# Optimization experiments

Hardware: AMD Instinct MI355X
Metric: run time of the kernel (lower is better)

## Reference

```python
import jax, jax.numpy as jnp
import numpy as np

B, S, D = 2, 1024, 768
H, DH = 12, 64
M = 64            # performer random features
DFF = 4 * D
EPS_LN = 1e-5
EPS_PHI = 1e-6


def setup_inputs() -> dict:
    key = jax.random.key(0)
    ks = jax.random.split(key, 12)
    std = 0.02
    return {
        "x": jax.random.normal(ks[0], (B, S, D), jnp.float32),
        "ln1_g": jnp.ones((D,), jnp.float32),
        "ln1_b": jnp.zeros((D,), jnp.float32),
        "w_attn": jax.random.normal(ks[1], (D, 3 * D), jnp.float32) * std,
        "b_attn": jnp.zeros((3 * D,), jnp.float32),
        "w_feat": jax.random.normal(ks[2], (M, DH), jnp.float32),  # FAVOR+ projection
        "w_proj": jax.random.normal(ks[3], (D, D), jnp.float32) * std,
        "b_proj": jnp.zeros((D,), jnp.float32),
        "ln2_g": jnp.ones((D,), jnp.float32),
        "ln2_b": jnp.zeros((D,), jnp.float32),
        "w_fc": jax.random.normal(ks[4], (D, DFF), jnp.float32) * std,
        "b_fc": jnp.zeros((DFF,), jnp.float32),
        "w_out": jax.random.normal(ks[5], (DFF, D), jnp.float32) * std,
        "b_out": jnp.zeros((D,), jnp.float32),
    }


def _layernorm(x, g, b):
    mu = jnp.mean(x, axis=-1, keepdims=True)
    var = jnp.mean(jnp.square(x - mu), axis=-1, keepdims=True)
    return (x - mu) * jax.lax.rsqrt(var + EPS_LN) * g + b


def _phi(x, w_feat):
    # FAVOR+ positive softmax-kernel features. x: [B,H,S,DH] (already scaled by dh^-1/4)
    proj = jnp.einsum('bhsd,md->bhsm', x, w_feat)
    sq = 0.5 * jnp.sum(jnp.square(x), axis=-1, keepdims=True)
    return jnp.exp(proj - sq) / np.sqrt(M) + EPS_PHI


def _performer_attn(q, k, v, w_feat, w_proj, b_proj):
    # split heads: [B,S,D] -> [B,H,S,DH]
    def heads(t):
        return t.reshape(B, S, H, DH).transpose(0, 2, 1, 3)
    q, k, v = heads(q), heads(k), heads(v)
    scale = DH ** -0.25
    phi_q = _phi(q * scale, w_feat)  # [B,H,S,M]
    phi_k = _phi(k * scale, w_feat)
    # causal linear attention via prefix sums
    kv = jnp.cumsum(phi_k[..., :, None] * v[..., None, :], axis=2)  # [B,H,S,M,DH]
    num = jnp.einsum('bhsm,bhsmd->bhsd', phi_q, kv)
    den = jnp.einsum('bhsm,bhsm->bhs', phi_q, jnp.cumsum(phi_k, axis=2))
    out = num / den[..., None]
    out = out.transpose(0, 2, 1, 3).reshape(B, S, D)
    return out @ w_proj + b_proj


def reference(x, ln1_g, ln1_b, w_attn, b_attn, w_feat, w_proj, b_proj,
              ln2_g, ln2_b, w_fc, b_fc, w_out, b_out):
    a = _layernorm(x, ln1_g, ln1_b)
    qkv = a @ w_attn + b_attn                      # TFConv1D
    q, k, v = jnp.split(qkv, 3, axis=2)
    x = x + _performer_attn(q, k, v, w_feat, w_proj, b_proj)
    m = _layernorm(x, ln2_g, ln2_b)
    m = jax.nn.gelu(m @ w_fc + b_fc, approximate=True) @ w_out + b_out
    return x + m
```

## Files before the change

kernel.cpp:

```cpp
#include <hip/hip_runtime.h>
#include <hip/hip_bf16.h>
#include <math.h>

#define BB 2
#define SS 1024
#define DD 768
#define HH 12
#define DHH 64
#define MM 64
#define DFF 3072
#define BS (BB*SS)
#define EPS_LN 1e-5f
#define EPS_PHI 1e-6f
#define CC 64
#define NC (SS/CC)
#define NQ 3840
#define PQOFF 2304
#define PKOFF 3072
#define VOFF  1536

typedef __hip_bfloat16 bf16;
using v8s = __attribute__((ext_vector_type(8))) short;
using v4f = __attribute__((ext_vector_type(4))) float;
struct b4 { bf16 v[4]; };

typedef const __attribute__((address_space(1))) void ga_void;
typedef __attribute__((address_space(3))) void ls_void;
__device__ __forceinline__ void gload16(const void* g, void* l) {
    __builtin_amdgcn_global_load_lds((ga_void*)g, (ls_void*)l, 16, 0, 0);
}

__global__ __launch_bounds__(256) void feat_kernel(const float* __restrict__ w_attn,
                                                   const float* __restrict__ b_attn,
                                                   const float* __restrict__ wfeat,
                                                   bf16* __restrict__ wext_t,
                                                   float* __restrict__ bias_ext) {
    __shared__ float wfTm[64][68];
    __shared__ float Wt[64][68];
    int bid = blockIdx.x;
    int t = threadIdx.x;
    if (bid == 288) {
        for (int i = t; i < 3 * DD; i += 256) bias_ext[i] = b_attn[i];
        return;
    }
    int jb = bid % 12, h = (bid / 12) % 12, isK = bid / 144;
    int j0 = jb * 64;
    int base = isK * DD + h * DHH;
    const float scale = 0.35355339059327373f;
    #pragma unroll
    for (int it = 0; it < 4; it++) {
        int fidx = it * 256 + t;
        int r = fidx >> 4, dc = (fidx & 15) * 4;
        float4 wv = *(const float4*)&wfeat[r * DHH + dc];
        wfTm[r][dc + 0] = scale * wv.x; wfTm[r][dc + 1] = scale * wv.y;
        wfTm[r][dc + 2] = scale * wv.z; wfTm[r][dc + 3] = scale * wv.w;
        float4 av = *(const float4*)&w_attn[(size_t)(j0 + r) * (3 * DD) + base + dc];
        Wt[r][dc + 0] = av.x; Wt[r][dc + 1] = av.y;
        Wt[r][dc + 2] = av.z; Wt[r][dc + 3] = av.w;
    }
    __syncthreads();
    int jl = t & 63, mg = (t >> 6) * 16;
    v4f acc[16];
    #pragma unroll
    for (int mi = 0; mi < 16; mi++) acc[mi] = {0.f, 0.f, 0.f, 0.f};
    #pragma unroll
    for (int dc = 0; dc < 16; dc++) {
        v4f wv = *(const v4f*)&Wt[jl][dc * 4];
        #pragma unroll
        for (int mi = 0; mi < 16; mi++) {
            v4f fv = *(const v4f*)&wfTm[mg + mi][dc * 4];
            acc[mi] += fv * wv;
        }
    }
    #pragma unroll
    for (int mi = 0; mi < 16; mi++) {
        float s = acc[mi][0] + acc[mi][1] + acc[mi][2] + acc[mi][3];
        wext_t[(size_t)(PQOFF + isK * DD + h * DHH + mg + mi) * DD + j0 + jl] = __float2bfloat16(s);
    }
    if (jb == 0 && t < 64) {
        float accb = 0.f;
        #pragma unroll 8
        for (int d = 0; d < 64; d++) accb += wfTm[t][d] * b_attn[base + d];
        bias_ext[PQOFF + isK * DD + h * DHH + t] = accb;
    }
}

__global__ __launch_bounds__(256) void prep_main(const float* __restrict__ x,
                                                 const float* __restrict__ ln1_g,
                                                 const float* __restrict__ ln1_b,
                                                 const float* __restrict__ w_attn,
                                                 const float* __restrict__ w_proj,
                                                 const float* __restrict__ w_fc,
                                                 const float* __restrict__ w_out,
                                                 bf16* __restrict__ a_bf,
                                                 bf16* __restrict__ wext_t,
                                                 bf16* __restrict__ wproj_t,
                                                 bf16* __restrict__ wfc_t,
                                                 bf16* __restrict__ wout_t) {
    __shared__ float smem[64 * 65];
    int bid = blockIdx.x;
    int t = threadIdx.x;
    if (bid < 2048) {
        int row = bid;
        const float* xr = x + (size_t)row * DD;
        float v0 = xr[t], v1 = xr[t + 256], v2 = xr[t + 512];
        float s = v0 + v1 + v2;
        float s2 = v0 * v0 + v1 * v1 + v2 * v2;
        #pragma unroll
        for (int off = 32; off > 0; off >>= 1) {
            s  += __shfl_xor(s,  off, 64);
            s2 += __shfl_xor(s2, off, 64);
        }
        float* ls = smem; float* ls2 = smem + 4;
        if ((t & 63) == 0) { ls[t >> 6] = s; ls2[t >> 6] = s2; }
        __syncthreads();
        s  = ls[0] + ls[1] + ls[2] + ls[3];
        s2 = ls2[0] + ls2[1] + ls2[2] + ls2[3];
        float mu  = s * (1.0f / DD);
        float var = s2 * (1.0f / DD) - mu * mu;
        float r = rsqrtf(var + EPS_LN);
        bf16* orow = a_bf + (size_t)row * DD;
        orow[t]       = __float2bfloat16((v0 - mu) * r * ln1_g[t]       + ln1_b[t]);
        orow[t + 256] = __float2bfloat16((v1 - mu) * r * ln1_g[t + 256] + ln1_b[t + 256]);
        orow[t + 512] = __float2bfloat16((v2 - mu) * r * ln1_g[t + 512] + ln1_b[t + 512]);
    } else {
        int b = bid - 2048;
        const float* in; bf16* outp; int K, N, xt, yt;
        if (b < 432)       { in = w_attn; outp = wext_t;  K = 768;  N = 2304; xt = b % 36; yt = b / 36; }
        else if (b < 576)  { int b1 = b - 432;  in = w_proj; outp = wproj_t; K = 768;  N = 768;  xt = b1 % 12; yt = b1 / 12; }
        else if (b < 1152) { int b1 = b - 576;  in = w_fc;   outp = wfc_t;   K = 768;  N = 3072; xt = b1 % 48; yt = b1 / 48; }
        else               { int b1 = b - 1152; in = w_out;  outp = wout_t;  K = 3072; N = 768;  xt = b1 % 12; yt = b1 / 12; }
        float (*sm)[65] = (float(*)[65])smem;
        int n0 = xt * 64, k0 = yt * 64;
        int rr = t >> 4, cc = (t & 15) * 4;
        #pragma unroll
        for (int it = 0; it < 4; it++) {
            int kr = it * 16 + rr;
            float4 v = *(const float4*)&in[(size_t)(k0 + kr) * N + n0 + cc];
            sm[kr][cc + 0] = v.x; sm[kr][cc + 1] = v.y;
            sm[kr][cc + 2] = v.z; sm[kr][cc + 3] = v.w;
        }
        __syncthreads();
        #pragma unroll
        for (int it = 0; it < 4; it++) {
            int nr = it * 16 + rr;
            b4 o;
            #pragma unroll
            for (int j = 0; j < 4; j++) o.v[j] = __float2bfloat16(sm[cc + j][nr]);
            *(b4*)&outp[(size_t)(n0 + nr) * K + k0 + cc] = o;
        }
    }
}

__global__ __launch_bounds__(256) void ln_kernel(const float* __restrict__ x,
                                                 const float* __restrict__ g,
                                                 const float* __restrict__ bta,
                                                 bf16* __restrict__ out) {
    int row = blockIdx.x;
    int t = threadIdx.x;
    const float* xr = x + (size_t)row * DD;
    float v0 = xr[t], v1 = xr[t + 256], v2 = xr[t + 512];
    float s = v0 + v1 + v2;
    float s2 = v0 * v0 + v1 * v1 + v2 * v2;
    #pragma unroll
    for (int off = 32; off > 0; off >>= 1) {
        s  += __shfl_xor(s,  off, 64);
        s2 += __shfl_xor(s2, off, 64);
    }
    __shared__ float ls[4], ls2[4];
    if ((t & 63) == 0) { ls[t >> 6] = s; ls2[t >> 6] = s2; }
    __syncthreads();
    s  = ls[0] + ls[1] + ls[2] + ls[3];
    s2 = ls2[0] + ls2[1] + ls2[2] + ls2[3];
    float mu  = s * (1.0f / DD);
    float var = s2 * (1.0f / DD) - mu * mu;
    float r = rsqrtf(var + EPS_LN);
    bf16* orow = out + (size_t)row * DD;
    orow[t]       = __float2bfloat16((v0 - mu) * r * g[t]       + bta[t]);
    orow[t + 256] = __float2bfloat16((v1 - mu) * r * g[t + 256] + bta[t + 256]);
    orow[t + 512] = __float2bfloat16((v2 - mu) * r * g[t + 512] + bta[t + 512]);
}

__device__ inline void swizzle44(int bid, int nx4, int& bx, int& by) {
    int g = bid >> 4, r = bid & 15;
    bx = (g % nx4) * 4 + (r & 3);
    by = (g / nx4) * 4 + (r >> 2);
}

__device__ inline float gelu_tanh(float x) {
    float x3 = x * x * x;
    float u = 0.7978845608028654f * (x + 0.044715f * x3);
    return 0.5f * x * (1.0f + tanhf(u));
}

template <int ACT, int HAS_RES, int OUT_BF16, int SQMODE>
__global__ __launch_bounds__(256) void gemm_k128(const bf16* __restrict__ A,
                                                 const bf16* __restrict__ BT,
                                                 const float* __restrict__ bias,
                                                 const float* __restrict__ res,
                                                 void* __restrict__ Cout,
                                                 int N, int K, int nx4,
                                                 float* __restrict__ sqbuf) {
    __shared__ bf16 Asl[64][128];
    __shared__ bf16 Bsl[64][128];
    int bx, by;
    swizzle44(blockIdx.x, nx4, bx, by);
    int tid = threadIdx.x;
    int m0 = by * 64, n0 = bx * 64;
    int wave = tid >> 6, lane = tid & 63;
    int qm = lane & 15, quad = lane >> 4;
    int srow = lane >> 4;
    int chnk = lane & 15;
    int sce = (chnk ^ srow) * 8;
    int sco = (chnk ^ (srow + 4)) * 8;
    const bf16* ag = A  + (size_t)(m0 + wave * 16 + srow) * K;
    const bf16* bg = BT + (size_t)(n0 + wave * 16 + srow) * K;
    int xr = (qm & 7) << 3;

    v4f acc[4] = {{0.f,0.f,0.f,0.f},{0.f,0.f,0.f,0.f},{0.f,0.f,0.f,0.f},{0.f,0.f,0.f,0.f}};

    for (int k0 = 0; k0 < K; k0 += 128) {
        __syncthreads();
        #pragma unroll
        for (int i = 0; i < 4; i++) {
            int sc = (i & 1) ? sco : sce;
            gload16(ag + (size_t)(4 * i) * K + k0 + sc, &Asl[wave * 16 + 4 * i][0]);
            gload16(bg + (size_t)(4 * i) * K + k0 + sc, &Bsl[wave * 16 + 4 * i][0]);
        }
        __syncthreads();
        #pragma unroll
        for (int kc = 0; kc < 4; kc++) {
            v8s a = *(const v8s*)&Asl[wave * 16 + qm][(kc * 32 + quad * 8) ^ xr];
            #pragma unroll
            for (int n = 0; n < 4; n++) {
                v8s b = *(const v8s*)&Bsl[n * 16 + qm][(kc * 32 + quad * 8) ^ xr];
                acc[n] = __builtin_amdgcn_mfma_f32_16x16x32_bf16(a, b, acc[n], 0, 0, 0);
            }
        }
    }

    int col_l = lane & 15;
    if (SQMODE && n0 < 1536) {
        int hidx = n0 >> 6;
        #pragma unroll
        for (int r = 0; r < 4; r++) {
            float hsq = 0.f;
            #pragma unroll
            for (int t2 = 0; t2 < 4; t2++) {
                float v = acc[t2][r] + bias[n0 + t2 * 16 + col_l];
                hsq += v * v;
            }
            hsq += __shfl_xor(hsq, 1, 64); hsq += __shfl_xor(hsq, 2, 64);
            hsq += __shfl_xor(hsq, 4, 64); hsq += __shfl_xor(hsq, 8, 64);
            if (col_l == 0) {
                int row = m0 + wave * 16 + quad * 4 + r;
                sqbuf[row * 24 + hidx] = hsq * (1.0f / 16.0f);
            }
        }
        return;
    }
    #pragma unroll
    for (int t2 = 0; t2 < 4; t2++) {
        int col = n0 + t2 * 16 + col_l;
        float bcol = bias[col];
        #pragma unroll
        for (int r = 0; r < 4; r++) {
            int row = m0 + wave * 16 + quad * 4 + r;
            float v = acc[t2][r] + bcol;
            if (ACT == 1) v = gelu_tanh(v);
            if (HAS_RES) v += res[(size_t)row * N + col];
            if (OUT_BF16) ((bf16*)Cout)[(size_t)row * N + col] = __float2bfloat16(v);
            else          ((float*)Cout)[(size_t)row * N + col] = v;
        }
    }
}

template <int ACT, int HAS_RES, int OUT_BF16>
__global__ __launch_bounds__(256) void gemm_m32_k128(const bf16* __restrict__ A,
                                                     const bf16* __restrict__ BT,
                                                     const float* __restrict__ bias,
                                                     const float* __restrict__ res,
                                                     void* __restrict__ Cout,
                                                     int N, int K, int nx4) {
    __shared__ bf16 Asl[32][128];
    __shared__ bf16 Bsl[64][128];
    int bx, by;
    swizzle44(blockIdx.x, nx4, bx, by);
    int tid = threadIdx.x;
    int m0 = by * 32, n0 = bx * 64;
    int wave = tid >> 6, lane = tid & 63;
    int qm = lane & 15, quad = lane >> 4;
    int rowh = (wave & 1) * 16;
    int colh = (wave >> 1) * 32;
    int srow = lane >> 4;
    int chnk = lane & 15;
    int sce = (chnk ^ srow) * 8;
    int sco = (chnk ^ (srow + 4)) * 8;
    const bf16* ag = A  + (size_t)(m0 + wave * 8  + srow) * K;
    const bf16* bg = BT + (size_t)(n0 + wave * 16 + srow) * K;
    int xr = (qm & 7) << 3;

    v4f acc[2] = {{0.f,0.f,0.f,0.f},{0.f,0.f,0.f,0.f}};

    for (int k0 = 0; k0 < K; k0 += 128) {
        __syncthreads();
        #pragma unroll
        for (int i = 0; i < 2; i++) {
            int sc = (i & 1) ? sco : sce;
            gload16(ag + (size_t)(4 * i) * K + k0 + sc, &Asl[wave * 8 + 4 * i][0]);
        }
        #pragma unroll
        for (int i = 0; i < 4; i++) {
            int sc = (i & 1) ? sco : sce;
            gload16(bg + (size_t)(4 * i) * K + k0 + sc, &Bsl[wave * 16 + 4 * i][0]);
        }
        __syncthreads();
        #pragma unroll
        for (int kc = 0; kc < 4; kc++) {
            v8s a  = *(const v8s*)&Asl[rowh + qm][(kc * 32 + quad * 8) ^ xr];
            v8s b0 = *(const v8s*)&Bsl[colh + qm][(kc * 32 + quad * 8) ^ xr];
            v8s b1 = *(const v8s*)&Bsl[colh + 16 + qm][(kc * 32 + quad * 8) ^ xr];
            acc[0] = __builtin_amdgcn_mfma_f32_16x16x32_bf16(a, b0, acc[0], 0, 0, 0);
            acc[1] = __builtin_amdgcn_mfma_f32_16x16x32_bf16(a, b1, acc[1], 0, 0, 0);
        }
    }

    #pragma unroll
    for (int ct = 0; ct < 2; ct++) {
        int col = n0 + colh + ct * 16 + qm;
        float bcol = bias[col];
        #pragma unroll
        for (int r = 0; r < 4; r++) {
            int row = m0 + rowh + quad * 4 + r;
            float v = acc[ct][r] + bcol;
            if (ACT == 1) v = gelu_tanh(v);
            if (HAS_RES) v += res[(size_t)row * N + col];
            if (OUT_BF16) ((bf16*)Cout)[(size_t)row * N + col] = __float2bfloat16(v);
            else          ((float*)Cout)[(size_t)row * N + col] = v;
        }
    }
}

__global__ __launch_bounds__(256) void scan_sums_mfma(const bf16* __restrict__ qkvp,
                                                      const float* __restrict__ sqbuf,
                                                      float* __restrict__ StateT,
                                                      float* __restrict__ Sk) {
    int c = blockIdx.x, h = blockIdx.y, b = blockIdx.z;
    int bh = b * HH + h;
    int t = threadIdx.x;
    __shared__ bf16 vt[64][72];
    __shared__ bf16 kt[64][72];
    int sr = t >> 4, cq = (t & 15) * 4;
    #pragma unroll
    for (int i = 0; i < 4; i++) {
        int s = sr + 16 * i;
        size_t grow = (size_t)b * SS + c * CC + s;
        size_t rowg = grow * NQ + h * DHH;
        b4 vv = *(const b4*)&qkvp[rowg + VOFF  + cq];
        b4 kp = *(const b4*)&qkvp[rowg + PKOFF + cq];
        float sq = sqbuf[grow * 24 + 12 + h];
        #pragma unroll
        for (int j = 0; j < 4; j++) {
            vt[cq + j][s] = vv.v[j];
            kt[cq + j][s] = __float2bfloat16(
                __expf(__bfloat162float(kp.v[j]) - sq) * 0.125f + EPS_PHI);
        }
    }
    __syncthreads();
    int wave = t >> 6, lane = t & 63, qm = lane & 15, quad = lane >> 4;
    v4f acc[4] = {{0.f,0.f,0.f,0.f},{0.f,0.f,0.f,0.f},{0.f,0.f,0.f,0.f},{0.f,0.f,0.f,0.f}};
    #pragma unroll
    for (int k0 = 0; k0 < 64; k0 += 32) {
        v8s a = *(const v8s*)&vt[wave * 16 + qm][k0 + quad * 8];
        #pragma unroll
        for (int n = 0; n < 4; n++) {
            v8s bb = *(const v8s*)&kt[n * 16 + qm][k0 + quad * 8];
            acc[n] = __builtin_amdgcn_mfma_f32_16x16x32_bf16(a, bb, acc[n], 0, 0, 0);
        }
    }
    float* dst = StateT + ((size_t)bh * NC + c) * 4096;
    int col_l = lane & 15;
    #pragma unroll
    for (int n = 0; n < 4; n++)
        #pragma unroll
        for (int r = 0; r < 4; r++) {
            int d = wave * 16 + quad * 4 + r;
            dst[d * 64 + n * 16 + col_l] = acc[n][r];
        }
    {
        int m = t >> 2, j = t & 3;
        float sum = 0.f;
        #pragma unroll
        for (int i2 = 0; i2 < 16; i2++) sum += __bfloat162float(kt[m][j * 16 + i2]);
        sum += __shfl_xor(sum, 1, 64);
        sum += __shfl_xor(sum, 2, 64);
        if (j == 0) Sk[((size_t)bh * NC + c) * 64 + m] = sum;
    }
}

__global__ __launch_bounds__(256) void scan_prefix_kernel(float* __restrict__ Skv,
                                                          float* __restrict__ Sk) {
    int bh = blockIdx.y;
    int t = blockIdx.x * 256 + threadIdx.x;
    size_t base = (size_t)bh * NC * 4096 + t;
    float acc = 0.f;
    for (int c = 0; c < NC; c++) {
        float v = Skv[base + (size_t)c * 4096];
        Skv[base + (size_t)c * 4096] = acc;
        acc += v;
    }
    if (blockIdx.x == 0 && threadIdx.x < 64) {
        size_t b2 = (size_t)bh * NC * 64 + threadIdx.x;
        float a2 = 0.f;
        for (int c = 0; c < NC; c++) {
            float v = Sk[b2 + (size_t)c * 64];
            Sk[b2 + (size_t)c * 64] = a2;
            a2 += v;
        }
    }
}

__global__ __launch_bounds__(256) void scan_chunk_mfma(const bf16* __restrict__ qkvp,
                                                       const float* __restrict__ sqbuf,
                                                       const float* __restrict__ StateT,
                                                       const float* __restrict__ SkPre,
                                                       bf16* __restrict__ attn) {
    int c = blockIdx.x, h = blockIdx.y, b = blockIdx.z;
    int bh = b * HH + h;
    int t = threadIdx.x;
    __shared__ bf16 qs[64][72];
    __shared__ bf16 ks[64][72];
    __shared__ bf16 vt[64][72];
    __shared__ bf16 stl[64][72];
    __shared__ bf16 P[64][72];
    int sr = t >> 4, cq = (t & 15) * 4;
    const float* stg = StateT + ((size_t)bh * NC + c) * 4096;
    #pragma unroll
    for (int i = 0; i < 4; i++) {
        int s = sr + 16 * i;
        size_t grow = (size_t)b * SS + c * CC + s;
        size_t rowg = grow * NQ + h * DHH;
        b4 qp = *(const b4*)&qkvp[rowg + PQOFF + cq];
        b4 kp = *(const b4*)&qkvp[rowg + PKOFF + cq];
        b4 vv = *(const b4*)&qkvp[rowg + VOFF  + cq];
        float4 sv = *(const float4*)&stg[s * 64 + cq];
        float sqq = sqbuf[grow * 24 + h];
        float sqk = sqbuf[grow * 24 + 12 + h];
        #pragma unroll
        for (int j = 0; j < 4; j++) {
            qs[s][cq + j] = __float2bfloat16(
                __expf(__bfloat162float(qp.v[j]) - sqq) * 0.125f + EPS_PHI);
            ks[s][cq + j] = __float2bfloat16(
                __expf(__bfloat162float(kp.v[j]) - sqk) * 0.125f + EPS_PHI);
            vt[cq + j][s] = vv.v[j];
        }
        stl[s][cq + 0] = __float2bfloat16(sv.x);
        stl[s][cq + 1] = __float2bfloat16(sv.y);
        stl[s][cq + 2] = __float2bfloat16(sv.z);
        stl[s][cq + 3] = __float2bfloat16(sv.w);
    }
    __syncthreads();
    int wave = t >> 6, lane = t & 63, qm = lane & 15, quad = lane >> 4;
    int col_l = lane & 15;
    int row0 = wave * 16;

    v4f a1[4] = {{0.f,0.f,0.f,0.f},{0.f,0.f,0.f,0.f},{0.f,0.f,0.f,0.f},{0.f,0.f,0.f,0.f}};
    #pragma unroll
    for (int k0 = 0; k0 < 64; k0 += 32) {
        v8s a = *(const v8s*)&qs[row0 + qm][k0 + quad * 8];
        #pragma unroll
        for (int n = 0; n < 4; n++) {
            v8s bb = *(const v8s*)&ks[n * 16 + qm][k0 + quad * 8];
            a1[n] = __builtin_amdgcn_mfma_f32_16x16x32_bf16(a, bb, a1[n], 0, 0, 0);
        }
    }
    float denl[4] = {0.f, 0.f, 0.f, 0.f};
    #pragma unroll
    for (int n = 0; n < 4; n++)
        #pragma unroll
        for (int r = 0; r < 4; r++) {
            int row = row0 + quad * 4 + r;
            int col = n * 16 + col_l;
            float v = (col <= row) ? a1[n][r] : 0.f;
            P[row][col] = __float2bfloat16(v);
            denl[r] += v;
        }
    {
        const float* skp = SkPre + ((size_t)bh * NC + c) * 64;
        float4 sk4 = *(const float4*)&skp[qm * 4];
        #pragma unroll
        for (int r = 0; r < 4; r++) {
            int row = row0 + quad * 4 + r;
            b4 qv = *(const b4*)&qs[row][qm * 4];
            denl[r] += __bfloat162float(qv.v[0]) * sk4.x
                     + __bfloat162float(qv.v[1]) * sk4.y
                     + __bfloat162float(qv.v[2]) * sk4.z
                     + __bfloat162float(qv.v[3]) * sk4.w;
        }
    }
    #pragma unroll
    for (int r = 0; r < 4; r++) {
        denl[r] += __shfl_xor(denl[r], 1, 64);
        denl[r] += __shfl_xor(denl[r], 2, 64);
        denl[r] += __shfl_xor(denl[r], 4, 64);
        denl[r] += __shfl_xor(denl[r], 8, 64);
    }
    v4f acc[4] = {{0.f,0.f,0.f,0.f},{0.f,0.f,0.f,0.f},{0.f,0.f,0.f,0.f},{0.f,0.f,0.f,0.f}};
    #pragma unroll
    for (int k0 = 0; k0 < 64; k0 += 32) {
        v8s aq = *(const v8s*)&qs[row0 + qm][k0 + quad * 8];
        v8s ap = *(const v8s*)&P [row0 + qm][k0 + quad * 8];
        #pragma unroll
        for (int n = 0; n < 4; n++) {
            v8s b1 = *(const v8s*)&stl[n * 16 + qm][k0 + quad * 8];
            v8s b2 = *(const v8s*)&vt [n * 16 + qm][k0 + quad * 8];
            acc[n] = __builtin_amdgcn_mfma_f32_16x16x32_bf16(aq, b1, acc[n], 0, 0, 0);
            acc[n] = __builtin_amdgcn_mfma_f32_16x16x32_bf16(ap, b2, acc[n], 0, 0, 0);
        }
    }
    #pragma unroll
    for (int n = 0; n < 4; n++)
        #pragma unroll
        for (int r = 0; r < 4; r++) {
            int srow = row0 + quad * 4 + r;
            int d = n * 16 + col_l;
            attn[((size_t)b * SS + c * CC + srow) * DD + h * DHH + d] =
                __float2bfloat16(acc[n][r] / denl[r]);
        }
}

extern "C" void kernel_launch(void* const* d_in, const int* in_sizes, int n_in,
                              void* d_out, int out_size, void* d_ws, size_t ws_size,
                              hipStream_t stream) {
    const float* x      = (const float*)d_in[0];
    const float* ln1_g  = (const float*)d_in[1];
    const float* ln1_b  = (const float*)d_in[2];
    const float* w_attn = (const float*)d_in[3];
    const float* b_attn = (const float*)d_in[4];
    const float* w_feat = (const float*)d_in[5];
    const float* w_proj = (const float*)d_in[6];
    const float* b_proj = (const float*)d_in[7];
    const float* ln2_g  = (const float*)d_in[8];
    const float* ln2_b  = (const float*)d_in[9];
    const float* w_fc   = (const float*)d_in[10];
    const float* b_fc   = (const float*)d_in[11];
    const float* w_out  = (const float*)d_in[12];
    const float* b_out  = (const float*)d_in[13];
    float* out = (float*)d_out;

    float* ws = (float*)d_ws;
    size_t off = 0;
    float* buf_x1   = ws + off; off += (size_t)BS * DD;
    float* buf_sk   = ws + off; off += (size_t)BB * HH * NC * MM;
    float* bias_ext = ws + off; off += NQ;
    float* buf_sq   = ws + off; off += (size_t)BS * 24;
    bf16* wb = (bf16*)(ws + off);
    size_t boff = 0;
    bf16* buf_qkvp    = wb + boff; boff += (size_t)BS * NQ;
    bf16* buf_a_bf    = wb + boff; boff += (size_t)BS * DD;
    bf16* buf_attn_bf = wb + boff; boff += (size_t)BS * DD;
    bf16* wext_t      = wb + boff; boff += (size_t)NQ * DD;
    bf16* wproj_t     = wb + boff; boff += (size_t)DD * DD;
    bf16* wfc_t       = wb + boff; boff += (size_t)DFF * DD;
    bf16* wout_t      = wb + boff; boff += (size_t)DD * DFF;
    float* buf_skv   = buf_x1;
    bf16*  buf_fc_bf = buf_qkvp;

    feat_kernel<<<289, 256, 0, stream>>>(w_attn, b_attn, w_feat, wext_t, bias_ext);
    prep_main<<<3776, 256, 0, stream>>>(x, ln1_g, ln1_b,
                                        w_attn, w_proj, w_fc, w_out,
                                        buf_a_bf, wext_t, wproj_t, wfc_t, wout_t);
    gemm_k128<0, 0, 1, 1><<<1920, 256, 0, stream>>>(
        buf_a_bf, wext_t, bias_ext, nullptr, buf_qkvp, NQ, DD, 15, buf_sq);
    scan_sums_mfma<<<dim3(NC, HH, BB), 256, 0, stream>>>(buf_qkvp, buf_sq, buf_skv, buf_sk);
    scan_prefix_kernel<<<dim3(4096 / 256, BB * HH), 256, 0, stream>>>(buf_skv, buf_sk);
    scan_chunk_mfma<<<dim3(NC, HH, BB), 256, 0, stream>>>(
        buf_qkvp, buf_sq, buf_skv, buf_sk, buf_attn_bf);
    gemm_m32_k128<0, 1, 0><<<768, 256, 0, stream>>>(
        buf_attn_bf, wproj_t, b_proj, x, buf_x1, DD, DD, 3);
    ln_kernel<<<BS, 256, 0, stream>>>(buf_x1, ln2_g, ln2_b, buf_a_bf);
    gemm_k128<1, 0, 1, 0><<<1536, 256, 0, stream>>>(
        buf_a_bf, wfc_t, b_fc, nullptr, buf_fc_bf, DFF, DD, 12, nullptr);
    gemm_m32_k128<0, 1, 0><<<768, 256, 0, stream>>>(
        buf_fc_bf, wout_t, b_out, buf_x1, out, DD, DFF, 3);
}
```

Measured before the change: 211.4 us.

## Use 2x2 wave tiling in GEMM and fuse chunk prefix scan via last-block atomic

The 64x64 GEMM tile is now split into a 2x2 grid of 32x32 wave subtiles, so each wave loads two A and two B fragments per k-step instead of one A and four B. This cuts LDS reads per MFMA. Because each wave now covers only half a head's columns, the squared-norm side buffer stores two partial sums per head, and the consumers add them. Separately, the standalone prefix-scan kernel is removed: the last chunk block of each (batch, head), found with an atomic counter and threadfences, does the sequential prefix over chunk states itself. This saves a launch but puts a serial 16-chunk scan on a single block per head.

```diff
diff --git a/kernel.cpp b/kernel.cpp
--- a/kernel.cpp
+++ b/kernel.cpp
@@ -34,13 +34,15 @@
                                                    const float* __restrict__ b_attn,
                                                    const float* __restrict__ wfeat,
                                                    bf16* __restrict__ wext_t,
-                                                   float* __restrict__ bias_ext) {
+                                                   float* __restrict__ bias_ext,
+                                                   int* __restrict__ cnt) {
     __shared__ float wfTm[64][68];
     __shared__ float Wt[64][68];
     int bid = blockIdx.x;
     int t = threadIdx.x;
     if (bid == 288) {
         for (int i = t; i < 3 * DD; i += 256) bias_ext[i] = b_attn[i];
+        if (t < BB * HH) cnt[t] = 0;
         return;
     }
     int jb = bid % 12, h = (bid / 12) % 12, isK = bid / 144;
@@ -216,8 +218,10 @@
     const bf16* ag = A  + (size_t)(m0 + wave * 16 + srow) * K;
     const bf16* bg = BT + (size_t)(n0 + wave * 16 + srow) * K;
     int xr = (qm & 7) << 3;
-
-    v4f acc[4] = {{0.f,0.f,0.f,0.f},{0.f,0.f,0.f,0.f},{0.f,0.f,0.f,0.f},{0.f,0.f,0.f,0.f}};
+    int wr = (wave & 1) * 32, wc = (wave >> 1) * 32;
+
+    v4f acc[2][2] = {{{0.f,0.f,0.f,0.f},{0.f,0.f,0.f,0.f}},
+                     {{0.f,0.f,0.f,0.f},{0.f,0.f,0.f,0.f}}};
 
     for (int k0 = 0; k0 < K; k0 += 128) {
         __syncthreads();
@@ -230,47 +234,57 @@
         __syncthreads();
         #pragma unroll
         for (int kc = 0; kc < 4; kc++) {
-            v8s a = *(const v8s*)&Asl[wave * 16 + qm][(kc * 32 + quad * 8) ^ xr];
-            #pragma unroll
-            for (int n = 0; n < 4; n++) {
-                v8s b = *(const v8s*)&Bsl[n * 16 + qm][(kc * 32 + quad * 8) ^ xr];
-                acc[n] = __builtin_amdgcn_mfma_f32_16x16x32_bf16(a, b, acc[n], 0, 0, 0);
-            }
+            int off = (kc * 32 + quad * 8) ^ xr;
+            v8s a0 = *(const v8s*)&Asl[wr + qm][off];
+            v8s a1 = *(const v8s*)&Asl[wr + 16 + qm][off];
+            v8s b0 = *(const v8s*)&Bsl[wc + qm][off];
+            v8s b1 = *(const v8s*)&Bsl[wc + 16 + qm][off];
+            acc[0][0] = __builtin_amdgcn_mfma_f32_16x16x32_bf16(a0, b0, acc[0][0], 0, 0, 0);
+            acc[0][1] = __builtin_amdgcn_mfma_f32_16x16x32_bf16(a0, b1, acc[0][1], 0, 0, 0);
+            acc[1][0] = __builtin_amdgcn_mfma_f32_16x16x32_bf16(a1, b0, acc[1][0], 0, 0, 0);
+            acc[1][1] = __builtin_amdgcn_mfma_f32_16x16x32_bf16(a1, b1, acc[1][1], 0, 0, 0);
         }
     }
 
     int col_l = lane & 15;
     if (SQMODE && n0 < 1536) {
         int hidx = n0 >> 6;
-        #pragma unroll
-        for (int r = 0; r < 4; r++) {
-            float hsq = 0.f;
+        int half = wc >> 5;
+        #pragma unroll
+        for (int m = 0; m < 2; m++) {
             #pragma unroll
-            for (int t2 = 0; t2 < 4; t2++) {
-                float v = acc[t2][r] + bias[n0 + t2 * 16 + col_l];
-                hsq += v * v;
+            for (int r = 0; r < 4; r++) {
+                float hsq = 0.f;
+                #pragma unroll
+                for (int n = 0; n < 2; n++) {
+                    float v = acc[m][n][r] + bias[n0 + wc + n * 16 + col_l];
+                    hsq += v * v;
+                }
+                hsq += __shfl_xor(hsq, 1, 64); hsq += __shfl_xor(hsq, 2, 64);
+                hsq += __shfl_xor(hsq, 4, 64); hsq += __shfl_xor(hsq, 8, 64);
+                if (col_l == 0) {
+                    int row = m0 + wr + m * 16 + quad * 4 + r;
+                    sqbuf[(size_t)row * 48 + hidx * 2 + half] = hsq * (1.0f / 16.0f);
+                }
             }
-            hsq += __shfl_xor(hsq, 1, 64); hsq += __shfl_xor(hsq, 2, 64);
-            hsq += __shfl_xor(hsq, 4, 64); hsq += __shfl_xor(hsq, 8, 64);
-            if (col_l == 0) {
-                int row = m0 + wave * 16 + quad * 4 + r;
-                sqbuf[row * 24 + hidx] = hsq * (1.0f / 16.0f);
+        }
+        return;
+    }
+    #pragma unroll
+    for (int n = 0; n < 2; n++) {
+        int col = n0 + wc + n * 16 + col_l;
+        float bcol = bias[col];
+        #pragma unroll
+        for (int m = 0; m < 2; m++) {
+            #pragma unroll
+            for (int r = 0; r < 4; r++) {
+                int row = m0 + wr + m * 16 + quad * 4 + r;
+                float v = acc[m][n][r] + bcol;
+                if (ACT == 1) v = gelu_tanh(v);
+                if (HAS_RES) v += res[(size_t)row * N + col];
+                if (OUT_BF16) ((bf16*)Cout)[(size_t)row * N + col] = __float2bfloat16(v);
+                else          ((float*)Cout)[(size_t)row * N + col] = v;
             }
-        }
-        return;
-    }
-    #pragma unroll
-    for (int t2 = 0; t2 < 4; t2++) {
-        int col = n0 + t2 * 16 + col_l;
-        float bcol = bias[col];
-        #pragma unroll
-        for (int r = 0; r < 4; r++) {
-            int row = m0 + wave * 16 + quad * 4 + r;
-            float v = acc[t2][r] + bcol;
-            if (ACT == 1) v = gelu_tanh(v);
-            if (HAS_RES) v += res[(size_t)row * N + col];
-            if (OUT_BF16) ((bf16*)Cout)[(size_t)row * N + col] = __float2bfloat16(v);
-            else          ((float*)Cout)[(size_t)row * N + col] = v;
         }
     }
 }
@@ -344,12 +358,14 @@
 __global__ __launch_bounds__(256) void scan_sums_mfma(const bf16* __restrict__ qkvp,
                                                       const float* __restrict__ sqbuf,
                                                       float* __restrict__ StateT,
-                                                      float* __restrict__ Sk) {
+                                                      float* __restrict__ Sk,
+                                                      int* __restrict__ cnt) {
     int c = blockIdx.x, h = blockIdx.y, b = blockIdx.z;
     int bh = b * HH + h;
     int t = threadIdx.x;
     __shared__ bf16 vt[64][72];
     __shared__ bf16 kt[64][72];
+    __shared__ int lastFlag;
     int sr = t >> 4, cq = (t & 15) * 4;
     #pragma unroll
     for (int i = 0; i < 4; i++) {
@@ -358,7 +374,7 @@
         size_t rowg = grow * NQ + h * DHH;
         b4 vv = *(const b4*)&qkvp[rowg + VOFF  + cq];
         b4 kp = *(const b4*)&qkvp[rowg + PKOFF + cq];
-        float sq = sqbuf[grow * 24 + 12 + h];
+        float sq = sqbuf[grow * 48 + 24 + h * 2] + sqbuf[grow * 48 + 24 + h * 2 + 1];
         #pragma unroll
         for (int j = 0; j < 4; j++) {
             vt[cq + j][s] = vv.v[j];
@@ -396,25 +412,34 @@
         sum += __shfl_xor(sum, 2, 64);
         if (j == 0) Sk[((size_t)bh * NC + c) * 64 + m] = sum;
     }
-}
-
-__global__ __launch_bounds__(256) void scan_prefix_kernel(float* __restrict__ Skv,
-                                                          float* __restrict__ Sk) {
-    int bh = blockIdx.y;
-    int t = blockIdx.x * 256 + threadIdx.x;
-    size_t base = (size_t)bh * NC * 4096 + t;
-    float acc = 0.f;
-    for (int c = 0; c < NC; c++) {
-        float v = Skv[base + (size_t)c * 4096];
-        Skv[base + (size_t)c * 4096] = acc;
-        acc += v;
-    }
-    if (blockIdx.x == 0 && threadIdx.x < 64) {
-        size_t b2 = (size_t)bh * NC * 64 + threadIdx.x;
+    __threadfence();
+    if (t == 0) {
+        int old = atomicAdd(&cnt[bh], 1);
+        lastFlag = (old == NC - 1);
+    }
+    __syncthreads();
+    if (!lastFlag) return;
+    __threadfence();
+    float* base = StateT + (size_t)bh * NC * 4096;
+    float accp[16];
+    #pragma unroll
+    for (int i = 0; i < 16; i++) accp[i] = 0.f;
+    for (int c2 = 0; c2 < NC; c2++) {
+        float v[16];
+        #pragma unroll
+        for (int i = 0; i < 16; i++) v[i] = base[(size_t)c2 * 4096 + t + i * 256];
+        #pragma unroll
+        for (int i = 0; i < 16; i++) {
+            base[(size_t)c2 * 4096 + t + i * 256] = accp[i];
+            accp[i] += v[i];
+        }
+    }
+    if (t < 64) {
+        size_t b2 = (size_t)bh * NC * 64 + t;
         float a2 = 0.f;
-        for (int c = 0; c < NC; c++) {
-            float v = Sk[b2 + (size_t)c * 64];
-            Sk[b2 + (size_t)c * 64] = a2;
+        for (int c2 = 0; c2 < NC; c2++) {
+            float v = Sk[b2 + (size_t)c2 * 64];
+            Sk[b2 + (size_t)c2 * 64] = a2;
             a2 += v;
         }
     }
@@ -444,8 +469,8 @@
         b4 kp = *(const b4*)&qkvp[rowg + PKOFF + cq];
         b4 vv = *(const b4*)&qkvp[rowg + VOFF  + cq];
         float4 sv = *(const float4*)&stg[s * 64 + cq];
-        float sqq = sqbuf[grow * 24 + h];
-        float sqk = sqbuf[grow * 24 + 12 + h];
+        float sqq = sqbuf[grow * 48 + h * 2]      + sqbuf[grow * 48 + h * 2 + 1];
+        float sqk = sqbuf[grow * 48 + 24 + h * 2] + sqbuf[grow * 48 + 24 + h * 2 + 1];
         #pragma unroll
         for (int j = 0; j < 4; j++) {
             qs[s][cq + j] = __float2bfloat16(
@@ -553,7 +578,8 @@
     float* buf_x1   = ws + off; off += (size_t)BS * DD;
     float* buf_sk   = ws + off; off += (size_t)BB * HH * NC * MM;
     float* bias_ext = ws + off; off += NQ;
-    float* buf_sq   = ws + off; off += (size_t)BS * 24;
+    float* buf_sq   = ws + off; off += (size_t)BS * 48;
+    int*   buf_cnt  = (int*)(ws + off); off += 32;
     bf16* wb = (bf16*)(ws + off);
     size_t boff = 0;
     bf16* buf_qkvp    = wb + boff; boff += (size_t)BS * NQ;
@@ -566,14 +592,14 @@
     float* buf_skv   = buf_x1;
     bf16*  buf_fc_bf = buf_qkvp;
 
-    feat_kernel<<<289, 256, 0, stream>>>(w_attn, b_attn, w_feat, wext_t, bias_ext);
+    feat_kernel<<<289, 256, 0, stream>>>(w_attn, b_attn, w_feat, wext_t, bias_ext, buf_cnt);
     prep_main<<<3776, 256, 0, stream>>>(x, ln1_g, ln1_b,
                                         w_attn, w_proj, w_fc, w_out,
                                         buf_a_bf, wext_t, wproj_t, wfc_t, wout_t);
     gemm_k128<0, 0, 1, 1><<<1920, 256, 0, stream>>>(
         buf_a_bf, wext_t, bias_ext, nullptr, buf_qkvp, NQ, DD, 15, buf_sq);
-    scan_sums_mfma<<<dim3(NC, HH, BB), 256, 0, stream>>>(buf_qkvp, buf_sq, buf_skv, buf_sk);
-    scan_prefix_kernel<<<dim3(4096 / 256, BB * HH), 256, 0, stream>>>(buf_skv, buf_sk);
+    scan_sums_mfma<<<dim3(NC, HH, BB), 256, 0, stream>>>(
+        buf_qkvp, buf_sq, buf_skv, buf_sk, buf_cnt);
     scan_chunk_mfma<<<dim3(NC, HH, BB), 256, 0, stream>>>(
         buf_qkvp, buf_sq, buf_skv, buf_sk, buf_attn_bf);
     gemm_m32_k128<0, 1, 0><<<768, 256, 0, stream>>>(
```

Result: slower. 272.0 us (+28.7%).

## Use 2x2 wave tiling in the 64x64 GEMM to cut LDS fragment reads

Applied to the files above, without the earlier changes.

The GEMM's four waves now each compute a 32x32 quadrant of the 64x64 tile using a 2x2 grid of MFMA accumulators. Before, each wave computed a 16x64 strip. Per k-chunk this needs 4 LDS fragment loads for 4 MFMAs instead of 5, so LDS traffic drops. Because each wave now covers only half of a head's columns, the sum-of-squares epilogue writes two partial sums per head into a buffer twice as wide. The scan and attention kernels add the two halves when they read it.

```diff
diff --git a/kernel.cpp b/kernel.cpp
--- a/kernel.cpp
+++ b/kernel.cpp
@@ -216,8 +216,10 @@
     const bf16* ag = A  + (size_t)(m0 + wave * 16 + srow) * K;
     const bf16* bg = BT + (size_t)(n0 + wave * 16 + srow) * K;
     int xr = (qm & 7) << 3;
-
-    v4f acc[4] = {{0.f,0.f,0.f,0.f},{0.f,0.f,0.f,0.f},{0.f,0.f,0.f,0.f},{0.f,0.f,0.f,0.f}};
+    int wr = (wave & 1) * 32, wc = (wave >> 1) * 32;
+
+    v4f acc[2][2] = {{{0.f,0.f,0.f,0.f},{0.f,0.f,0.f,0.f}},
+                     {{0.f,0.f,0.f,0.f},{0.f,0.f,0.f,0.f}}};
 
     for (int k0 = 0; k0 < K; k0 += 128) {
         __syncthreads();
@@ -230,47 +232,57 @@
         __syncthreads();
         #pragma unroll
         for (int kc = 0; kc < 4; kc++) {
-            v8s a = *(const v8s*)&Asl[wave * 16 + qm][(kc * 32 + quad * 8) ^ xr];
-            #pragma unroll
-            for (int n = 0; n < 4; n++) {
-                v8s b = *(const v8s*)&Bsl[n * 16 + qm][(kc * 32 + quad * 8) ^ xr];
-                acc[n] = __builtin_amdgcn_mfma_f32_16x16x32_bf16(a, b, acc[n], 0, 0, 0);
-            }
+            int off = (kc * 32 + quad * 8) ^ xr;
+            v8s a0 = *(const v8s*)&Asl[wr + qm][off];
+            v8s a1 = *(const v8s*)&Asl[wr + 16 + qm][off];
+            v8s b0 = *(const v8s*)&Bsl[wc + qm][off];
+            v8s b1 = *(const v8s*)&Bsl[wc + 16 + qm][off];
+            acc[0][0] = __builtin_amdgcn_mfma_f32_16x16x32_bf16(a0, b0, acc[0][0], 0, 0, 0);
+            acc[0][1] = __builtin_amdgcn_mfma_f32_16x16x32_bf16(a0, b1, acc[0][1], 0, 0, 0);
+            acc[1][0] = __builtin_amdgcn_mfma_f32_16x16x32_bf16(a1, b0, acc[1][0], 0, 0, 0);
+            acc[1][1] = __builtin_amdgcn_mfma_f32_16x16x32_bf16(a1, b1, acc[1][1], 0, 0, 0);
         }
     }
 
     int col_l = lane & 15;
     if (SQMODE && n0 < 1536) {
         int hidx = n0 >> 6;
-        #pragma unroll
-        for (int r = 0; r < 4; r++) {
-            float hsq = 0.f;
+        int half = wc >> 5;
+        #pragma unroll
+        for (int m = 0; m < 2; m++) {
             #pragma unroll
-            for (int t2 = 0; t2 < 4; t2++) {
-                float v = acc[t2][r] + bias[n0 + t2 * 16 + col_l];
-                hsq += v * v;
+            for (int r = 0; r < 4; r++) {
+                float hsq = 0.f;
+                #pragma unroll
+                for (int n = 0; n < 2; n++) {
+                    float v = acc[m][n][r] + bias[n0 + wc + n * 16 + col_l];
+                    hsq += v * v;
+                }
+                hsq += __shfl_xor(hsq, 1, 64); hsq += __shfl_xor(hsq, 2, 64);
+                hsq += __shfl_xor(hsq, 4, 64); hsq += __shfl_xor(hsq, 8, 64);
+                if (col_l == 0) {
+                    int row = m0 + wr + m * 16 + quad * 4 + r;
+                    sqbuf[(size_t)row * 48 + hidx * 2 + half] = hsq * (1.0f / 16.0f);
+                }
             }
-            hsq += __shfl_xor(hsq, 1, 64); hsq += __shfl_xor(hsq, 2, 64);
-            hsq += __shfl_xor(hsq, 4, 64); hsq += __shfl_xor(hsq, 8, 64);
-            if (col_l == 0) {
-                int row = m0 + wave * 16 + quad * 4 + r;
-                sqbuf[row * 24 + hidx] = hsq * (1.0f / 16.0f);
+        }
+        return;
+    }
+    #pragma unroll
+    for (int n = 0; n < 2; n++) {
+        int col = n0 + wc + n * 16 + col_l;
+        float bcol = bias[col];
+        #pragma unroll
+        for (int m = 0; m < 2; m++) {
+            #pragma unroll
+            for (int r = 0; r < 4; r++) {
+                int row = m0 + wr + m * 16 + quad * 4 + r;
+                float v = acc[m][n][r] + bcol;
+                if (ACT == 1) v = gelu_tanh(v);
+                if (HAS_RES) v += res[(size_t)row * N + col];
+                if (OUT_BF16) ((bf16*)Cout)[(size_t)row * N + col] = __float2bfloat16(v);
+                else          ((float*)Cout)[(size_t)row * N + col] = v;
             }
-        }
-        return;
-    }
-    #pragma unroll
-    for (int t2 = 0; t2 < 4; t2++) {
-        int col = n0 + t2 * 16 + col_l;
-        float bcol = bias[col];
-        #pragma unroll
-        for (int r = 0; r < 4; r++) {
-            int row = m0 + wave * 16 + quad * 4 + r;
-            float v = acc[t2][r] + bcol;
-            if (ACT == 1) v = gelu_tanh(v);
-            if (HAS_RES) v += res[(size_t)row * N + col];
-            if (OUT_BF16) ((bf16*)Cout)[(size_t)row * N + col] = __float2bfloat16(v);
-            else          ((float*)Cout)[(size_t)row * N + col] = v;
         }
     }
 }
@@ -358,7 +370,7 @@
         size_t rowg = grow * NQ + h * DHH;
         b4 vv = *(const b4*)&qkvp[rowg + VOFF  + cq];
         b4 kp = *(const b4*)&qkvp[rowg + PKOFF + cq];
-        float sq = sqbuf[grow * 24 + 12 + h];
+        float sq = sqbuf[grow * 48 + 24 + h * 2] + sqbuf[grow * 48 + 24 + h * 2 + 1];
         #pragma unroll
         for (int j = 0; j < 4; j++) {
             vt[cq + j][s] = vv.v[j];
@@ -444,8 +456,8 @@
         b4 kp = *(const b4*)&qkvp[rowg + PKOFF + cq];
         b4 vv = *(const b4*)&qkvp[rowg + VOFF  + cq];
         float4 sv = *(const float4*)&stg[s * 64 + cq];
-        float sqq = sqbuf[grow * 24 + h];
-        float sqk = sqbuf[grow * 24 + 12 + h];
+        float sqq = sqbuf[grow * 48 + h * 2]      + sqbuf[grow * 48 + h * 2 + 1];
+        float sqk = sqbuf[grow * 48 + 24 + h * 2] + sqbuf[grow * 48 + 24 + h * 2 + 1];
         #pragma unroll
         for (int j = 0; j < 4; j++) {
             qs[s][cq + j] = __float2bfloat16(
@@ -553,7 +565,7 @@
     float* buf_x1   = ws + off; off += (size_t)BS * DD;
     float* buf_sk   = ws + off; off += (size_t)BB * HH * NC * MM;
     float* bias_ext = ws + off; off += NQ;
-    float* buf_sq   = ws + off; off += (size_t)BS * 24;
+    float* buf_sq   = ws + off; off += (size_t)BS * 48;
     bf16* wb = (bf16*)(ws + off);
     size_t boff = 0;
     bf16* buf_qkvp    = wb + boff; boff += (size_t)BS * NQ;
```

Result: no change. 210.2 us, median of 2 (-0.5%).
